# Performance work log

Hardware: AMD Instinct MI355X
Metric: run time of the kernel (lower is better)

## Reference

```python
import jax, jax.numpy as jnp
import numpy as np

EPS = 1e-8  # torch CosineSimilarity default eps

def _mlp2(h, W1, b1, W2, b2):
    # two-layer MLP with ReLU after each linear
    h = jax.nn.relu(h @ W1 + b1)
    return jax.nn.relu(h @ W2 + b2)

def setup_inputs() -> dict:
    key = jax.random.key(0)
    ks = jax.random.split(key, 24)
    N, E, D, O, P = 65536, 131072, 256, 128, 32
    inp = {
        "x": jax.random.normal(ks[0], (N, D), dtype=jnp.float32),
        "edge_index": jax.random.randint(ks[1], (2, E), 0, N, dtype=jnp.int64),
        "edge_attr": jax.random.normal(ks[2], (E, P), dtype=jnp.float32),
    }
    sD = 1.0 / np.sqrt(D)
    for i, name in enumerate(["1", "2", "3", "4"]):
        inp[f"W{name}a"] = jax.random.normal(ks[3 + 4 * i], (D, D), dtype=jnp.float32) * sD
        inp[f"b{name}a"] = jnp.zeros((D,), dtype=jnp.float32)
        inp[f"W{name}b"] = jax.random.normal(ks[4 + 4 * i], (D, O), dtype=jnp.float32) * sD
        inp[f"b{name}b"] = jnp.zeros((O,), dtype=jnp.float32)
    Fin = 1 + 4 * O + P  # 545
    inp["Wf"] = jax.random.normal(ks[20], (Fin, O), dtype=jnp.float32) / np.sqrt(Fin)
    inp["bf"] = jnp.zeros((O,), dtype=jnp.float32)
    return inp

def reference(x, edge_index, edge_attr,
              W1a, b1a, W1b, b1b,
              W2a, b2a, W2b, b2b,
              W3a, b3a, W3b, b3b,
              W4a, b4a, W4b, b4b,
              Wf, bf):
    x_src = x[edge_index[0]]  # [E, D]
    x_dst = x[edge_index[1]]  # [E, D]
    y = jnp.concatenate([
        _mlp2(x_src, W1a, b1a, W1b, b1b),
        _mlp2(x_dst, W2a, b2a, W2b, b2b),
        _mlp2(x_src - x_dst, W3a, b3a, W3b, b3b),
        _mlp2(x_src * x_dst, W4a, b4a, W4b, b4b),
    ], axis=1)  # [E, 4*O]
    # cosine similarity over feature dim (torch dim=1 after unsqueeze(2)) -> [E, 1]
    ns = jnp.maximum(jnp.linalg.norm(x_src, axis=1, keepdims=True), EPS)
    nd = jnp.maximum(jnp.linalg.norm(x_dst, axis=1, keepdims=True), EPS)
    s = jnp.sum((x_src / ns) * (x_dst / nd), axis=1, keepdims=True)  # [E, 1]
    z = jnp.concatenate([y, s, edge_attr], axis=1)  # [E, 1+4*O+P]
    return jnp.tanh(z @ Wf + bf)  # [E, O]
```

## Files before the change

### kernel.cpp

```cpp
#include <hip/hip_runtime.h>
#include <hip/hip_bf16.h>

typedef unsigned short u16;
typedef __attribute__((ext_vector_type(8))) short short8;
typedef __attribute__((ext_vector_type(4))) float f32x4;

#define NE 131072

#define OFF_WA 0
#define OFF_WB 262144
#define OFF_WF 393216
#define OFF_WE 458752
#define OFF_WS 462848

#define ASYNC16(gp, lp) __builtin_amdgcn_global_load_lds( \
    (const __attribute__((address_space(1))) unsigned int*)(gp), \
    (__attribute__((address_space(3))) unsigned int*)(lp), 16, 0, 0)
#define LGKM0() __builtin_amdgcn_s_waitcnt(0xC07F)
#define WAIT4() asm volatile("s_waitcnt vmcnt(4)" ::: "memory")
#define WAIT2() asm volatile("s_waitcnt vmcnt(2)" ::: "memory")
#define WAIT0() asm volatile("s_waitcnt vmcnt(0)" ::: "memory")
#define BAR() asm volatile("s_waitcnt lgkmcnt(0)\n\ts_barrier" ::: "memory")

__device__ __forceinline__ float b2f(u16 v) {
    unsigned int u = ((unsigned int)v) << 16;
    float f;
    __builtin_memcpy(&f, &u, 4);
    return f;
}
__device__ __forceinline__ u16 f2b(float f) {
    __hip_bfloat16 h = __float2bfloat16(f);
    u16 u;
    __builtin_memcpy(&u, &h, 2);
    return u;
}
__device__ __forceinline__ short8 pack8(f32x4 a, f32x4 b) {
    short8 p;
    p[0] = (short)f2b(a.x); p[1] = (short)f2b(a.y);
    p[2] = (short)f2b(a.z); p[3] = (short)f2b(a.w);
    p[4] = (short)f2b(b.x); p[5] = (short)f2b(b.y);
    p[6] = (short)f2b(b.z); p[7] = (short)f2b(b.w);
    return p;
}

#define MFMA16(a, b, c) __builtin_amdgcn_mfma_f32_16x16x32_bf16(a, b, c, 0, 0, 0)

struct BiasP {
    const float* ba[4];
    const float* bb[4];
};

__device__ __forceinline__ void issue_chunk(const u16* __restrict__ ws, u16* Wb,
                                            int wave, int lane, int gc) {
    if (gc >= 112) return;
    const int m = gc / 28;
    const int c = gc - m * 28;
    const int r = lane >> 2;
    const int slot = (lane & 3) ^ ((lane >> 3) & 3);
    u16* lp = Wb + wave * 3072 + (gc % 3) * 1024;
    const u16* gp;
    int rstride;
    if (c < 16) {
        int kk = c >> 1, nh = c & 1;
        gp = ws + OFF_WA + m * 65536
           + (size_t)(wave * 64 + nh * 32 + r) * 256 + kk * 32 + slot * 8;
        rstride = 16 * 256;
    } else if (c < 24) {
        int kc = c - 16;
        gp = ws + OFF_WB + m * 32768
           + (size_t)(wave * 32 + r) * 256 + kc * 32 + slot * 8;
        rstride = 16 * 256;
    } else {
        int cc = c - 24;
        gp = ws + OFF_WF + m * 16384
           + (size_t)(wave * 32 + r) * 128 + cc * 32 + slot * 8;
        rstride = 16 * 128;
    }
    ASYNC16(gp, lp);
    ASYNC16(gp + rstride, lp + 512);
}

__global__ __launch_bounds__(256)
void prep_kernel(const float* __restrict__ W1a, const float* __restrict__ W2a,
                 const float* __restrict__ W3a, const float* __restrict__ W4a,
                 const float* __restrict__ W1b, const float* __restrict__ W2b,
                 const float* __restrict__ W3b, const float* __restrict__ W4b,
                 const float* __restrict__ Wf,  u16* __restrict__ ws) {
    __shared__ __align__(16) u16 T[64 * 80];

    const int y = blockIdx.y;
    const int t = threadIdx.x;
    const float* in;
    int K, N;
    if (y < 4)      { in = (y == 0) ? W1a : (y == 1) ? W2a : (y == 2) ? W3a : W4a; K = 256; N = 256; }
    else if (y < 8) { in = (y == 4) ? W1b : (y == 5) ? W2b : (y == 6) ? W3b : W4b; K = 256; N = 128; }
    else            { in = Wf; K = 545; N = 128; }

    const int ntilesN = N / 64;
    const int ktiles = (K + 63) / 64;
    const int kt = blockIdx.x / ntilesN;
    const int nt = blockIdx.x - kt * ntilesN;
    if (kt >= ktiles) return;
    const int kbase = kt * 64, nbase = nt * 64;

    {
        int tn = (t & 15) * 4;
        int tk = t >> 4;
        #pragma unroll
        for (int r = 0; r < 4; r++) {
            int k = kbase + tk + 16 * r;
            if (k < K) {
                float4 v = *(const float4*)(in + (size_t)k * N + nbase + tn);
                T[(tn + 0) * 80 + tk + 16 * r] = f2b(v.x);
                T[(tn + 1) * 80 + tk + 16 * r] = f2b(v.y);
                T[(tn + 2) * 80 + tk + 16 * r] = f2b(v.z);
                T[(tn + 3) * 80 + tk + 16 * r] = f2b(v.w);
            }
        }
    }
    __syncthreads();
    {
        int n = t >> 2;
        int kc = (t & 3) * 16;
        int n_out = nbase + n;
        const u16* src = &T[n * 80 + kc];
        if (y < 4) {
            u16* dst = ws + OFF_WA + y * 65536 + (size_t)n_out * 256 + kbase + kc;
            *(short8*)dst = *(const short8*)src;
            *(short8*)(dst + 8) = *(const short8*)(src + 8);
        } else if (y < 8) {
            u16* dst = ws + OFF_WB + (y - 4) * 32768 + (size_t)n_out * 256 + kbase + kc;
            *(short8*)dst = *(const short8*)src;
            *(short8*)(dst + 8) = *(const short8*)(src + 8);
        } else if (kbase < 512) {
            u16* dst = ws + OFF_WF + (kbase >> 7) * 16384 + (size_t)n_out * 128 + (kbase & 127) + kc;
            *(short8*)dst = *(const short8*)src;
            *(short8*)(dst + 8) = *(const short8*)(src + 8);
        } else {
            #pragma unroll
            for (int j = 0; j < 16; j++) {
                int k = kbase + kc + j;
                if (k < 545) {
                    u16 v = src[j];
                    if (k == 512)      ws[OFF_WS + n_out] = v;
                    else               ws[OFF_WE + n_out * 32 + (k - 513)] = v;
                }
            }
        }
    }
}

__global__ __launch_bounds__(256, 2)
void fused_kernel(const float* __restrict__ x, const int* __restrict__ ei,
                  const float* __restrict__ ea, const u16* __restrict__ ws,
                  BiasP bp, const float* __restrict__ bfp, float* __restrict__ out) {
    __shared__ __align__(16) u16 Xs[32][264];
    __shared__ __align__(16) u16 Xd[32][264];
    __shared__ __align__(16) u16 Hs[32][264];
    __shared__ __align__(16) u16 Wb[12288];
    __shared__ float scos[32];

    const int t = threadIdx.x;
    const int wave = t >> 6;
    const int lane = t & 63;
    const int l15 = lane & 15;
    const int g = lane >> 4;
    const int e0 = blockIdx.x * 32;
    const f32x4 zero4 = {0.f, 0.f, 0.f, 0.f};
    const int colA = wave * 64;
    const int colC = wave * 32;

    bool idx64 = true;
    #pragma unroll
    for (int i = 1; i < 16; i += 2) { idx64 = idx64 && (ei[i] == 0); }

    short8 eaA[2];
    #pragma unroll
    for (int mt = 0; mt < 2; mt++) {
        const float* er = ea + (size_t)(e0 + mt * 16 + l15) * 32 + g * 8;
        f32x4 a = *(const f32x4*)(er);
        f32x4 b = *(const f32x4*)(er + 4);
        eaA[mt] = pack8(a, b);
    }
    short8 eaB[2];
    float epi_b[2], epi_w[2];
    #pragma unroll
    for (int nt = 0; nt < 2; nt++) {
        int col = colC + nt * 16 + l15;
        eaB[nt] = *(const short8*)(ws + OFF_WE + col * 32 + g * 8);
        epi_b[nt] = bfp[col];
        epi_w[nt] = b2f(ws[OFF_WS + col]);
    }
    float biasA[4][4], biasB[4][2];
    #pragma unroll
    for (int m = 0; m < 4; m++) {
        #pragma unroll
        for (int nt = 0; nt < 4; nt++) biasA[m][nt] = bp.ba[m][colA + nt * 16 + l15];
        #pragma unroll
        for (int nt = 0; nt < 2; nt++) biasB[m][nt] = bp.bb[m][colC + nt * 16 + l15];
    }

    issue_chunk(ws, Wb, wave, lane, 0);
    issue_chunk(ws, Wb, wave, lane, 1);
    issue_chunk(ws, Wb, wave, lane, 2);

    {
        int edge = t >> 3;
        int c = t & 7;
        int pos = e0 + edge;
        int is = idx64 ? ei[2 * pos] : ei[pos];
        int id = idx64 ? ei[2 * (NE + pos)] : ei[NE + pos];
        const float* rs = x + (size_t)is * 256 + c * 32;
        const float* rd = x + (size_t)id * 256 + c * 32;
        float dot = 0.f, ss = 0.f, dd = 0.f;
        #pragma unroll
        for (int i = 0; i < 4; i++) {
            f32x4 s0 = *(const f32x4*)(rs + i * 8);
            f32x4 s1 = *(const f32x4*)(rs + i * 8 + 4);
            f32x4 d0 = *(const f32x4*)(rd + i * 8);
            f32x4 d1 = *(const f32x4*)(rd + i * 8 + 4);
            dot += s0.x * d0.x + s0.y * d0.y + s0.z * d0.z + s0.w * d0.w
                 + s1.x * d1.x + s1.y * d1.y + s1.z * d1.z + s1.w * d1.w;
            ss  += s0.x * s0.x + s0.y * s0.y + s0.z * s0.z + s0.w * s0.w
                 + s1.x * s1.x + s1.y * s1.y + s1.z * s1.z + s1.w * s1.w;
            dd  += d0.x * d0.x + d0.y * d0.y + d0.z * d0.z + d0.w * d0.w
                 + d1.x * d1.x + d1.y * d1.y + d1.z * d1.z + d1.w * d1.w;
            *(short8*)(&Xs[edge][c * 32 + i * 8]) = pack8(s0, s1);
            *(short8*)(&Xd[edge][c * 32 + i * 8]) = pack8(d0, d1);
        }
        dot += __shfl_xor(dot, 1); ss += __shfl_xor(ss, 1); dd += __shfl_xor(dd, 1);
        dot += __shfl_xor(dot, 2); ss += __shfl_xor(ss, 2); dd += __shfl_xor(dd, 2);
        dot += __shfl_xor(dot, 4); ss += __shfl_xor(ss, 4); dd += __shfl_xor(dd, 4);
        if (c == 0) {
            float ns = fmaxf(sqrtf(ss), 1e-8f);
            float nd = fmaxf(sqrtf(dd), 1e-8f);
            scos[edge] = dot / (ns * nd);
        }
    }
    BAR();

    const u16* xsb0 = &Xs[l15][g * 8];      const u16* xsb1 = &Xs[16 + l15][g * 8];
    const u16* xdb0 = &Xd[l15][g * 8];      const u16* xdb1 = &Xd[16 + l15][g * 8];
    const u16* hgb0 = &Hs[l15][g * 8];      const u16* hgb1 = &Hs[16 + l15][g * 8];
    const u16* wbase = Wb + wave * 3072 + l15 * 32 + ((g ^ ((l15 >> 1) & 3)) * 8);

    f32x4 Facc[2][2];
    #pragma unroll
    for (int a = 0; a < 2; a++) {
        #pragma unroll
        for (int b = 0; b < 2; b++) Facc[a][b] = zero4;
    }

    #pragma unroll
    for (int m = 0; m < 4; m++) {
        f32x4 accA[2][4];
        #pragma unroll
        for (int a = 0; a < 2; a++) {
            #pragma unroll
            for (int b = 0; b < 4; b++) accA[a][b] = zero4;
        }
        #pragma unroll
        for (int kk = 0; kk < 8; kk++) {
            const int gc = m * 28 + kk * 2;
            short8 s0, s1, d0, d1;
            if (m != 1) { s0 = *(const short8*)(xsb0 + kk * 32); s1 = *(const short8*)(xsb1 + kk * 32); }
            if (m != 0) { d0 = *(const short8*)(xdb0 + kk * 32); d1 = *(const short8*)(xdb1 + kk * 32); }
            WAIT4();
            const u16* wq0 = wbase + (gc % 3) * 1024;
            short8 wf0 = *(const short8*)(wq0);
            short8 wf1 = *(const short8*)(wq0 + 512);
            LGKM0();
            issue_chunk(ws, Wb, wave, lane, gc + 3);
            short8 af0, af1;
            if (m == 0)      { af0 = s0; af1 = s1; }
            else if (m == 1) { af0 = d0; af1 = d1; }
            else {
                #pragma unroll
                for (int mt = 0; mt < 2; mt++) {
                    short8 s = mt ? s1 : s0, d = mt ? d1 : d0, rr;
                    #pragma unroll
                    for (int j = 0; j < 8; j++) {
                        float fs = b2f((u16)s[j]);
                        float fd = b2f((u16)d[j]);
                        rr[j] = (short)f2b((m == 2) ? (fs - fd) : (fs * fd));
                    }
                    if (mt) af1 = rr; else af0 = rr;
                }
            }
            accA[0][0] = MFMA16(af0, wf0, accA[0][0]);
            accA[1][0] = MFMA16(af1, wf0, accA[1][0]);
            accA[0][1] = MFMA16(af0, wf1, accA[0][1]);
            accA[1][1] = MFMA16(af1, wf1, accA[1][1]);
            WAIT4();
            const u16* wq1 = wbase + ((gc + 1) % 3) * 1024;
            short8 wf2 = *(const short8*)(wq1);
            short8 wf3 = *(const short8*)(wq1 + 512);
            LGKM0();
            issue_chunk(ws, Wb, wave, lane, gc + 4);
            accA[0][2] = MFMA16(af0, wf2, accA[0][2]);
            accA[1][2] = MFMA16(af1, wf2, accA[1][2]);
            accA[0][3] = MFMA16(af0, wf3, accA[0][3]);
            accA[1][3] = MFMA16(af1, wf3, accA[1][3]);
        }
        #pragma unroll
        for (int nt = 0; nt < 4; nt++) {
            int col = colA + nt * 16 + l15;
            #pragma unroll
            for (int mt = 0; mt < 2; mt++) {
                #pragma unroll
                for (int rg = 0; rg < 4; rg++) {
                    int row = mt * 16 + g * 4 + rg;
                    Hs[row][col] = f2b(fmaxf(accA[mt][nt][rg] + biasA[m][nt], 0.f));
                }
            }
        }
        BAR();

        f32x4 accB[2][2];
        #pragma unroll
        for (int a = 0; a < 2; a++) {
            #pragma unroll
            for (int b = 0; b < 2; b++) accB[a][b] = zero4;
        }
        #pragma unroll
        for (int kc = 0; kc < 8; kc++) {
            const int gc = m * 28 + 16 + kc;
            short8 hf0 = *(const short8*)(hgb0 + kc * 32);
            short8 hf1 = *(const short8*)(hgb1 + kc * 32);
            WAIT4();
            const u16* wq = wbase + (gc % 3) * 1024;
            short8 wf0 = *(const short8*)(wq);
            short8 wf1 = *(const short8*)(wq + 512);
            LGKM0();
            issue_chunk(ws, Wb, wave, lane, gc + 3);
            accB[0][0] = MFMA16(hf0, wf0, accB[0][0]);
            accB[1][0] = MFMA16(hf1, wf0, accB[1][0]);
            accB[0][1] = MFMA16(hf0, wf1, accB[0][1]);
            accB[1][1] = MFMA16(hf1, wf1, accB[1][1]);
        }
        BAR();
        #pragma unroll
        for (int nt = 0; nt < 2; nt++) {
            int col = colC + nt * 16 + l15;
            #pragma unroll
            for (int mt = 0; mt < 2; mt++) {
                #pragma unroll
                for (int rg = 0; rg < 4; rg++) {
                    int row = mt * 16 + g * 4 + rg;
                    Hs[row][col] = f2b(fmaxf(accB[mt][nt][rg] + biasB[m][nt], 0.f));
                }
            }
        }
        BAR();

        #pragma unroll
        for (int cc = 0; cc < 4; cc++) {
            const int gc = m * 28 + 24 + cc;
            short8 gf0 = *(const short8*)(hgb0 + cc * 32);
            short8 gf1 = *(const short8*)(hgb1 + cc * 32);
            if (m == 3 && cc == 2)      { WAIT2(); }
            else if (m == 3 && cc == 3) { WAIT0(); }
            else                        { WAIT4(); }
            const u16* wq = wbase + (gc % 3) * 1024;
            short8 wf0 = *(const short8*)(wq);
            short8 wf1 = *(const short8*)(wq + 512);
            LGKM0();
            issue_chunk(ws, Wb, wave, lane, gc + 3);
            Facc[0][0] = MFMA16(gf0, wf0, Facc[0][0]);
            Facc[1][0] = MFMA16(gf1, wf0, Facc[1][0]);
            Facc[0][1] = MFMA16(gf0, wf1, Facc[0][1]);
            Facc[1][1] = MFMA16(gf1, wf1, Facc[1][1]);
        }
        if (m < 3) BAR();
    }

    #pragma unroll
    for (int mt = 0; mt < 2; mt++) {
        #pragma unroll
        for (int nt = 0; nt < 2; nt++) {
            Facc[mt][nt] = MFMA16(eaA[mt], eaB[nt], Facc[mt][nt]);
        }
    }

    float* os = (float*)&Xs[0][0];
    #pragma unroll
    for (int nt = 0; nt < 2; nt++) {
        int col = colC + nt * 16 + l15;
        #pragma unroll
        for (int mt = 0; mt < 2; mt++) {
            #pragma unroll
            for (int rg = 0; rg < 4; rg++) {
                int row = mt * 16 + g * 4 + rg;
                float v = Facc[mt][nt][rg] + scos[row] * epi_w[nt] + epi_b[nt];
                v = fminf(fmaxf(v, -15.f), 15.f);
                float e2 = __expf(2.f * v);
                os[row * 132 + col] = (e2 - 1.f) / (e2 + 1.f);
            }
        }
    }
    BAR();
    {
        int row = t >> 3, c = t & 7;
        float* op = out + (size_t)(e0 + row) * 128 + c * 16;
        const float* sp = os + row * 132 + c * 16;
        #pragma unroll
        for (int i = 0; i < 4; i++) {
            f32x4 v = *(const f32x4*)(sp + i * 4);
            *(f32x4*)(op + i * 4) = v;
        }
    }
}

extern "C" void kernel_launch(void* const* d_in, const int* in_sizes, int n_in,
                              void* d_out, int out_size, void* d_ws, size_t ws_size,
                              hipStream_t stream) {
    u16* ws = (u16*)d_ws;
    prep_kernel<<<dim3(18, 9), 256, 0, stream>>>(
        (const float*)d_in[3],  (const float*)d_in[7],  (const float*)d_in[11], (const float*)d_in[15],
        (const float*)d_in[5],  (const float*)d_in[9],  (const float*)d_in[13], (const float*)d_in[17],
        (const float*)d_in[19], ws);

    BiasP bp;
    bp.ba[0] = (const float*)d_in[4];  bp.ba[1] = (const float*)d_in[8];
    bp.ba[2] = (const float*)d_in[12]; bp.ba[3] = (const float*)d_in[16];
    bp.bb[0] = (const float*)d_in[6];  bp.bb[1] = (const float*)d_in[10];
    bp.bb[2] = (const float*)d_in[14]; bp.bb[3] = (const float*)d_in[18];

    fused_kernel<<<NE / 32, 256, 0, stream>>>(
        (const float*)d_in[0], (const int*)d_in[1], (const float*)d_in[2], ws,
        bp, (const float*)d_in[20], (float*)d_out);
}
```

Measured before the change: 421.5 us.

## Double edge tile per block to 64 to halve weight streaming per edge

Each block now processes 64 edges instead of 32, so every streamed weight chunk feeds four MFMA row tiles instead of two, halving total weight traffic from global memory into LDS. Shared buffers, accumulators, the gather and the output store are all widened to match, and the edge_attr and epilogue loads are moved after the main loop to ease register pressure. Launch bounds drop to one block per CU, which lowers occupancy and doubles accumulator registers, so there is less latency hiding for the irregular gathers.

```diff
diff --git a/kernel.cpp b/kernel.cpp
--- a/kernel.cpp
+++ b/kernel.cpp
@@ -150,22 +150,22 @@
     }
 }
 
-__global__ __launch_bounds__(256, 2)
+__global__ __launch_bounds__(256, 1)
 void fused_kernel(const float* __restrict__ x, const int* __restrict__ ei,
                   const float* __restrict__ ea, const u16* __restrict__ ws,
                   BiasP bp, const float* __restrict__ bfp, float* __restrict__ out) {
-    __shared__ __align__(16) u16 Xs[32][264];
-    __shared__ __align__(16) u16 Xd[32][264];
-    __shared__ __align__(16) u16 Hs[32][264];
+    __shared__ __align__(16) u16 Xs[64][264];
+    __shared__ __align__(16) u16 Xd[64][264];
+    __shared__ __align__(16) u16 Hs[64][264];
     __shared__ __align__(16) u16 Wb[12288];
-    __shared__ float scos[32];
+    __shared__ float scos[64];
 
     const int t = threadIdx.x;
     const int wave = t >> 6;
     const int lane = t & 63;
     const int l15 = lane & 15;
     const int g = lane >> 4;
-    const int e0 = blockIdx.x * 32;
+    const int e0 = blockIdx.x * 64;
     const f32x4 zero4 = {0.f, 0.f, 0.f, 0.f};
     const int colA = wave * 64;
     const int colC = wave * 32;
@@ -174,23 +174,6 @@
     #pragma unroll
     for (int i = 1; i < 16; i += 2) { idx64 = idx64 && (ei[i] == 0); }
 
-    short8 eaA[2];
-    #pragma unroll
-    for (int mt = 0; mt < 2; mt++) {
-        const float* er = ea + (size_t)(e0 + mt * 16 + l15) * 32 + g * 8;
-        f32x4 a = *(const f32x4*)(er);
-        f32x4 b = *(const f32x4*)(er + 4);
-        eaA[mt] = pack8(a, b);
-    }
-    short8 eaB[2];
-    float epi_b[2], epi_w[2];
-    #pragma unroll
-    for (int nt = 0; nt < 2; nt++) {
-        int col = colC + nt * 16 + l15;
-        eaB[nt] = *(const short8*)(ws + OFF_WE + col * 32 + g * 8);
-        epi_b[nt] = bfp[col];
-        epi_w[nt] = b2f(ws[OFF_WS + col]);
-    }
     float biasA[4][4], biasB[4][2];
     #pragma unroll
     for (int m = 0; m < 4; m++) {
@@ -205,16 +188,16 @@
     issue_chunk(ws, Wb, wave, lane, 2);
 
     {
-        int edge = t >> 3;
-        int c = t & 7;
+        int edge = t >> 2;
+        int c = t & 3;
         int pos = e0 + edge;
         int is = idx64 ? ei[2 * pos] : ei[pos];
         int id = idx64 ? ei[2 * (NE + pos)] : ei[NE + pos];
-        const float* rs = x + (size_t)is * 256 + c * 32;
-        const float* rd = x + (size_t)id * 256 + c * 32;
+        const float* rs = x + (size_t)is * 256 + c * 64;
+        const float* rd = x + (size_t)id * 256 + c * 64;
         float dot = 0.f, ss = 0.f, dd = 0.f;
         #pragma unroll
-        for (int i = 0; i < 4; i++) {
+        for (int i = 0; i < 8; i++) {
             f32x4 s0 = *(const f32x4*)(rs + i * 8);
             f32x4 s1 = *(const f32x4*)(rs + i * 8 + 4);
             f32x4 d0 = *(const f32x4*)(rd + i * 8);
@@ -225,12 +208,11 @@
                  + s1.x * s1.x + s1.y * s1.y + s1.z * s1.z + s1.w * s1.w;
             dd  += d0.x * d0.x + d0.y * d0.y + d0.z * d0.z + d0.w * d0.w
                  + d1.x * d1.x + d1.y * d1.y + d1.z * d1.z + d1.w * d1.w;
-            *(short8*)(&Xs[edge][c * 32 + i * 8]) = pack8(s0, s1);
-            *(short8*)(&Xd[edge][c * 32 + i * 8]) = pack8(d0, d1);
+            *(short8*)(&Xs[edge][c * 64 + i * 8]) = pack8(s0, s1);
+            *(short8*)(&Xd[edge][c * 64 + i * 8]) = pack8(d0, d1);
         }
         dot += __shfl_xor(dot, 1); ss += __shfl_xor(ss, 1); dd += __shfl_xor(dd, 1);
         dot += __shfl_xor(dot, 2); ss += __shfl_xor(ss, 2); dd += __shfl_xor(dd, 2);
-        dot += __shfl_xor(dot, 4); ss += __shfl_xor(ss, 4); dd += __shfl_xor(dd, 4);
         if (c == 0) {
             float ns = fmaxf(sqrtf(ss), 1e-8f);
             float nd = fmaxf(sqrtf(dd), 1e-8f);
@@ -239,74 +221,79 @@
     }
     BAR();
 
-    const u16* xsb0 = &Xs[l15][g * 8];      const u16* xsb1 = &Xs[16 + l15][g * 8];
-    const u16* xdb0 = &Xd[l15][g * 8];      const u16* xdb1 = &Xd[16 + l15][g * 8];
-    const u16* hgb0 = &Hs[l15][g * 8];      const u16* hgb1 = &Hs[16 + l15][g * 8];
+    const u16* xsb[4]; const u16* xdb[4]; const u16* hgb[4];
+    #pragma unroll
+    for (int mt = 0; mt < 4; mt++) {
+        xsb[mt] = &Xs[mt * 16 + l15][g * 8];
+        xdb[mt] = &Xd[mt * 16 + l15][g * 8];
+        hgb[mt] = &Hs[mt * 16 + l15][g * 8];
+    }
     const u16* wbase = Wb + wave * 3072 + l15 * 32 + ((g ^ ((l15 >> 1) & 3)) * 8);
 
-    f32x4 Facc[2][2];
-    #pragma unroll
-    for (int a = 0; a < 2; a++) {
+    f32x4 Facc[4][2];
+    #pragma unroll
+    for (int a = 0; a < 4; a++) {
         #pragma unroll
         for (int b = 0; b < 2; b++) Facc[a][b] = zero4;
     }
 
     #pragma unroll
     for (int m = 0; m < 4; m++) {
-        f32x4 accA[2][4];
-        #pragma unroll
-        for (int a = 0; a < 2; a++) {
+        f32x4 accA[4][4];
+        #pragma unroll
+        for (int a = 0; a < 4; a++) {
             #pragma unroll
             for (int b = 0; b < 4; b++) accA[a][b] = zero4;
         }
         #pragma unroll
         for (int kk = 0; kk < 8; kk++) {
             const int gc = m * 28 + kk * 2;
-            short8 s0, s1, d0, d1;
-            if (m != 1) { s0 = *(const short8*)(xsb0 + kk * 32); s1 = *(const short8*)(xsb1 + kk * 32); }
-            if (m != 0) { d0 = *(const short8*)(xdb0 + kk * 32); d1 = *(const short8*)(xdb1 + kk * 32); }
+            short8 af[4];
+            #pragma unroll
+            for (int mt = 0; mt < 4; mt++) {
+                if (m == 0)      af[mt] = *(const short8*)(xsb[mt] + kk * 32);
+                else if (m == 1) af[mt] = *(const short8*)(xdb[mt] + kk * 32);
+                else {
+                    short8 s = *(const short8*)(xsb[mt] + kk * 32);
+                    short8 d = *(const short8*)(xdb[mt] + kk * 32);
+                    short8 rr;
+                    #pragma unroll
+                    for (int j = 0; j < 8; j++) {
+                        float fs = b2f((u16)s[j]);
+                        float fd = b2f((u16)d[j]);
+                        rr[j] = (short)f2b((m == 2) ? (fs - fd) : (fs * fd));
+                    }
+                    af[mt] = rr;
+                }
+            }
             WAIT4();
             const u16* wq0 = wbase + (gc % 3) * 1024;
             short8 wf0 = *(const short8*)(wq0);
             short8 wf1 = *(const short8*)(wq0 + 512);
             LGKM0();
             issue_chunk(ws, Wb, wave, lane, gc + 3);
-            short8 af0, af1;
-            if (m == 0)      { af0 = s0; af1 = s1; }
-            else if (m == 1) { af0 = d0; af1 = d1; }
-            else {
-                #pragma unroll
-                for (int mt = 0; mt < 2; mt++) {
-                    short8 s = mt ? s1 : s0, d = mt ? d1 : d0, rr;
-                    #pragma unroll
-                    for (int j = 0; j < 8; j++) {
-                        float fs = b2f((u16)s[j]);
-                        float fd = b2f((u16)d[j]);
-                        rr[j] = (short)f2b((m == 2) ? (fs - fd) : (fs * fd));
-                    }
-                    if (mt) af1 = rr; else af0 = rr;
-                }
-            }
-            accA[0][0] = MFMA16(af0, wf0, accA[0][0]);
-            accA[1][0] = MFMA16(af1, wf0, accA[1][0]);
-            accA[0][1] = MFMA16(af0, wf1, accA[0][1]);
-            accA[1][1] = MFMA16(af1, wf1, accA[1][1]);
+            #pragma unroll
+            for (int mt = 0; mt < 4; mt++) {
+                accA[mt][0] = MFMA16(af[mt], wf0, accA[mt][0]);
+                accA[mt][1] = MFMA16(af[mt], wf1, accA[mt][1]);
+            }
             WAIT4();
             const u16* wq1 = wbase + ((gc + 1) % 3) * 1024;
             short8 wf2 = *(const short8*)(wq1);
             short8 wf3 = *(const short8*)(wq1 + 512);
             LGKM0();
             issue_chunk(ws, Wb, wave, lane, gc + 4);
-            accA[0][2] = MFMA16(af0, wf2, accA[0][2]);
-            accA[1][2] = MFMA16(af1, wf2, accA[1][2]);
-            accA[0][3] = MFMA16(af0, wf3, accA[0][3]);
-            accA[1][3] = MFMA16(af1, wf3, accA[1][3]);
+            #pragma unroll
+            for (int mt = 0; mt < 4; mt++) {
+                accA[mt][2] = MFMA16(af[mt], wf2, accA[mt][2]);
+                accA[mt][3] = MFMA16(af[mt], wf3, accA[mt][3]);
+            }
         }
         #pragma unroll
         for (int nt = 0; nt < 4; nt++) {
             int col = colA + nt * 16 + l15;
             #pragma unroll
-            for (int mt = 0; mt < 2; mt++) {
+            for (int mt = 0; mt < 4; mt++) {
                 #pragma unroll
                 for (int rg = 0; rg < 4; rg++) {
                     int row = mt * 16 + g * 4 + rg;
@@ -316,34 +303,36 @@
         }
         BAR();
 
-        f32x4 accB[2][2];
-        #pragma unroll
-        for (int a = 0; a < 2; a++) {
+        f32x4 accB[4][2];
+        #pragma unroll
+        for (int a = 0; a < 4; a++) {
             #pragma unroll
             for (int b = 0; b < 2; b++) accB[a][b] = zero4;
         }
         #pragma unroll
         for (int kc = 0; kc < 8; kc++) {
             const int gc = m * 28 + 16 + kc;
-            short8 hf0 = *(const short8*)(hgb0 + kc * 32);
-            short8 hf1 = *(const short8*)(hgb1 + kc * 32);
+            short8 hf[4];
+            #pragma unroll
+            for (int mt = 0; mt < 4; mt++) hf[mt] = *(const short8*)(hgb[mt] + kc * 32);
             WAIT4();
             const u16* wq = wbase + (gc % 3) * 1024;
             short8 wf0 = *(const short8*)(wq);
             short8 wf1 = *(const short8*)(wq + 512);
             LGKM0();
             issue_chunk(ws, Wb, wave, lane, gc + 3);
-            accB[0][0] = MFMA16(hf0, wf0, accB[0][0]);
-            accB[1][0] = MFMA16(hf1, wf0, accB[1][0]);
-            accB[0][1] = MFMA16(hf0, wf1, accB[0][1]);
-            accB[1][1] = MFMA16(hf1, wf1, accB[1][1]);
+            #pragma unroll
+            for (int mt = 0; mt < 4; mt++) {
+                accB[mt][0] = MFMA16(hf[mt], wf0, accB[mt][0]);
+                accB[mt][1] = MFMA16(hf[mt], wf1, accB[mt][1]);
+            }
         }
         BAR();
         #pragma unroll
         for (int nt = 0; nt < 2; nt++) {
             int col = colC + nt * 16 + l15;
             #pragma unroll
-            for (int mt = 0; mt < 2; mt++) {
+            for (int mt = 0; mt < 4; mt++) {
                 #pragma unroll
                 for (int rg = 0; rg < 4; rg++) {
                     int row = mt * 16 + g * 4 + rg;
@@ -356,8 +345,9 @@
         #pragma unroll
         for (int cc = 0; cc < 4; cc++) {
             const int gc = m * 28 + 24 + cc;
-            short8 gf0 = *(const short8*)(hgb0 + cc * 32);
-            short8 gf1 = *(const short8*)(hgb1 + cc * 32);
+            short8 gf[4];
+            #pragma unroll
+            for (int mt = 0; mt < 4; mt++) gf[mt] = *(const short8*)(hgb[mt] + cc * 32);
             if (m == 3 && cc == 2)      { WAIT2(); }
             else if (m == 3 && cc == 3) { WAIT0(); }
             else                        { WAIT4(); }
@@ -366,16 +356,33 @@
             short8 wf1 = *(const short8*)(wq + 512);
             LGKM0();
             issue_chunk(ws, Wb, wave, lane, gc + 3);
-            Facc[0][0] = MFMA16(gf0, wf0, Facc[0][0]);
-            Facc[1][0] = MFMA16(gf1, wf0, Facc[1][0]);
-            Facc[0][1] = MFMA16(gf0, wf1, Facc[0][1]);
-            Facc[1][1] = MFMA16(gf1, wf1, Facc[1][1]);
+            #pragma unroll
+            for (int mt = 0; mt < 4; mt++) {
+                Facc[mt][0] = MFMA16(gf[mt], wf0, Facc[mt][0]);
+                Facc[mt][1] = MFMA16(gf[mt], wf1, Facc[mt][1]);
+            }
         }
         if (m < 3) BAR();
     }
 
-    #pragma unroll
-    for (int mt = 0; mt < 2; mt++) {
+    short8 eaA[4], eaB[2];
+    float epi_b[2], epi_w[2];
+    #pragma unroll
+    for (int mt = 0; mt < 4; mt++) {
+        const float* er = ea + (size_t)(e0 + mt * 16 + l15) * 32 + g * 8;
+        f32x4 a = *(const f32x4*)(er);
+        f32x4 b = *(const f32x4*)(er + 4);
+        eaA[mt] = pack8(a, b);
+    }
+    #pragma unroll
+    for (int nt = 0; nt < 2; nt++) {
+        int col = colC + nt * 16 + l15;
+        eaB[nt] = *(const short8*)(ws + OFF_WE + col * 32 + g * 8);
+        epi_b[nt] = bfp[col];
+        epi_w[nt] = b2f(ws[OFF_WS + col]);
+    }
+    #pragma unroll
+    for (int mt = 0; mt < 4; mt++) {
         #pragma unroll
         for (int nt = 0; nt < 2; nt++) {
             Facc[mt][nt] = MFMA16(eaA[mt], eaB[nt], Facc[mt][nt]);
@@ -387,7 +394,7 @@
     for (int nt = 0; nt < 2; nt++) {
         int col = colC + nt * 16 + l15;
         #pragma unroll
-        for (int mt = 0; mt < 2; mt++) {
+        for (int mt = 0; mt < 4; mt++) {
             #pragma unroll
             for (int rg = 0; rg < 4; rg++) {
                 int row = mt * 16 + g * 4 + rg;
@@ -400,11 +407,11 @@
     }
     BAR();
     {
-        int row = t >> 3, c = t & 7;
-        float* op = out + (size_t)(e0 + row) * 128 + c * 16;
-        const float* sp = os + row * 132 + c * 16;
-        #pragma unroll
-        for (int i = 0; i < 4; i++) {
+        int row = t >> 2, c = t & 3;
+        float* op = out + (size_t)(e0 + row) * 128 + c * 32;
+        const float* sp = os + row * 132 + c * 32;
+        #pragma unroll
+        for (int i = 0; i < 8; i++) {
             f32x4 v = *(const f32x4*)(sp + i * 4);
             *(f32x4*)(op + i * 4) = v;
         }
@@ -426,7 +433,7 @@
     bp.bb[0] = (const float*)d_in[6];  bp.bb[1] = (const float*)d_in[10];
     bp.bb[2] = (const float*)d_in[14]; bp.bb[3] = (const float*)d_in[18];
 
-    fused_kernel<<<NE / 32, 256, 0, stream>>>(
+    fused_kernel<<<NE / 64, 256, 0, stream>>>(
         (const float*)d_in[0], (const int*)d_in[1], (const float*)d_in[2], ws,
         bp, (const float*)d_in[20], (float*)d_out);
 }
```

New measurement: 541.5 us. 28.5% more time.
